# Kernel optimization log

Measured on AMD Instinct MI355X. Metric: run time of the kernel, lower is better.

## Reference

```python
import jax, jax.numpy as jnp
import numpy as np

B = 65536          # batch
NUM_RULES = 4      # num_rules (init default)
NUM_VARS = 2       # effective num_variables after op-slot handling
RULE_DIM = 64
VAR_DIM = 100      # per-variable feature dim
HIDDEN_DIM = 2 * VAR_DIM  # 200, pinned by primary[:, :100] cat -> rule_mlp(hidden_dim)
D_K = 32           # variable_rule_select key dim
MLP_HID = 128      # GroupMLP hidden width


def _uniform(key, shape, fan_in):
    bound = 1.0 / np.sqrt(fan_in)
    return jax.random.uniform(key, shape, minval=-bound, maxval=bound, dtype=jnp.float32)


def setup_inputs() -> dict:
    key = jax.random.key(0)
    ks = jax.random.split(key, 7)
    return {
        "hidden": jax.random.normal(ks[0], (B, 3, VAR_DIM), dtype=jnp.float32),
        # rule embeddings: nn.Parameter(torch.randn(1, num_rules, rule_dim))
        "rule_emb": jax.random.normal(ks[1], (1, NUM_RULES, RULE_DIM), dtype=jnp.float32),
        # SelectAttention shared query (share_query=True -> nn.Linear(rule_dim, d_k))
        "Wq": _uniform(ks[2], (RULE_DIM, D_K), RULE_DIM),
        "bq": _uniform(ks[3], (D_K,), RULE_DIM),
        # SelectAttention per-variable key proj (GroupLinearLayer(hidden_dim, d_k, num_vars))
        "Wk": _uniform(ks[4], (NUM_VARS, HIDDEN_DIM, D_K), HIDDEN_DIM),
        # rule_mlp = GroupMLP(hidden_dim, hidden_dim//2, num_rules): two grouped linears
        "W1": _uniform(ks[5], (NUM_RULES, HIDDEN_DIM, MLP_HID), HIDDEN_DIM),
        "W2": _uniform(ks[6], (NUM_RULES, MLP_HID, VAR_DIM), MLP_HID),
    }


def argmax_onehot(x):
    # ArgMax.forward: scatter 1 at argmax along dim 1 (eval-mode hard selection)
    return jax.nn.one_hot(jnp.argmax(x, axis=1), x.shape[1], dtype=x.dtype)


def reference(hidden, rule_emb, Wq, bq, Wk, W1, W2):
    b = hidden.shape[0]
    # build operand representations: op slot broadcast onto both operands
    op = jnp.repeat(hidden[:, 2:3, :], NUM_VARS, axis=1)            # (B, 2, 100)
    h = jnp.concatenate([hidden[:, :NUM_VARS, :], op], axis=-1)    # (B, 2, 200)

    rule_e = jnp.broadcast_to(rule_emb, (b, NUM_RULES, RULE_DIM))   # (B, 4, 64)

    # SelectAttention(rule_emb, hidden): shared query linear, grouped key linear
    read = rule_e @ Wq + bq                                         # (B, 4, 32)
    write = jnp.einsum('bvd,vdk->bvk', h, Wk)                       # (B, 2, 32)
    scores = jnp.einsum('brk,bvk->brv', read, write) / jnp.sqrt(jnp.float32(D_K))  # (B,4,2)

    # eval path: hard ArgMax one-hot over flattened (rule, variable) pairs
    mask = argmax_onehot(scores.reshape(b, -1)).reshape(b, NUM_RULES, NUM_VARS)
    mask = jnp.transpose(mask, (0, 2, 1))                           # (B, vars, rules)

    variable_mask = jnp.sum(mask, axis=2, keepdims=True)            # (B, 2, 1)
    rule_mask = jnp.sum(mask, axis=1)[:, :, None]                   # (B, 4, 1)

    primary = jnp.sum(h * variable_mask, axis=1)                    # (B, 200)
    context = jnp.sum(h * (1.0 - variable_mask), axis=1)            # (B, 200)

    rule_mlp_input = jnp.concatenate(
        [primary[:, :VAR_DIM], context[:, :VAR_DIM]], axis=1)       # (B, 200)

    # grouped rule MLP applied per rule, then gated by rule_mask
    x = jnp.broadcast_to(rule_mlp_input[:, None, :], (b, NUM_RULES, HIDDEN_DIM))
    x = jax.nn.relu(jnp.einsum('bnd,ndk->bnk', x, W1))              # (B, 4, 128)
    x = jnp.einsum('bnd,ndk->bnk', x, W2)                           # (B, 4, 100)
    out = jnp.sum(x * rule_mask, axis=1)                            # (B, 100)
    return out
```

## Files before the change

kernel.cpp:

```cpp
#include <hip/hip_runtime.h>
#include <hip/hip_bf16.h>

#define B_TOTAL 65536
#define NR 4
#define VD 100
#define HD 200
#define DK 32
#define MH 128
#define RD 64

typedef __attribute__((ext_vector_type(8))) short bf16x8;
typedef __attribute__((ext_vector_type(4))) float f32x4;

static __device__ inline unsigned short f2bf(float x) {
    __hip_bfloat16 h = __float2bfloat16(x);
    return __builtin_bit_cast(unsigned short, h);
}

#define WS_GC    0
#define WS_CNT   19200
#define WS_LIST  19456
#define WS_VB    543744
#define WS_W1F   609280
#define WS_W2F   838656

__global__ __launch_bounds__(256) void k0_prep(
    const float* __restrict__ rule_emb, const float* __restrict__ Wq,
    const float* __restrict__ bq, const float* __restrict__ Wk,
    double* __restrict__ Gc, int* __restrict__ cnt)
{
    int tid = threadIdx.x;
    if (tid < NR) cnt[tid] = 0;

    __shared__ double readS[NR * DK];
    if (tid < NR * DK) {
        int r = tid >> 5, k = tid & 31;
        double a = (double)bq[k];
        for (int d = 0; d < RD; ++d)
            a += (double)rule_emb[r * RD + d] * (double)Wq[d * DK + k];
        readS[tid] = a;
    }
    __syncthreads();

    for (int idx = tid; idx < 100 * 16; idx += 256) {
        int dd = idx >> 4, c = idx & 15;
        int isB = (c >> 3) & 1, v = (c >> 2) & 1, r = c & 3;
        int row = v * HD + isB * 100 + dd;
        double g = 0.0;
        for (int k = 0; k < DK; ++k)
            g += (double)Wk[row * DK + k] * readS[r * DK + k];
        Gc[idx] = g;
    }
}

__global__ __launch_bounds__(256) void k0_wfrag(
    const float* __restrict__ W1, const float* __restrict__ W2,
    unsigned short* __restrict__ W1f, unsigned short* __restrict__ W2f)
{
    int i = blockIdx.x * 256 + threadIdx.x;
    if (i < 114688) {
        int r = i / 28672, rem = i % 28672;
        int ks = rem / 4096, rem2 = rem % 4096;
        int n = rem2 >> 9, l = (rem2 >> 3) & 63, j = rem2 & 7;
        int k = ks * 32 + ((l >> 4) << 3) + j;
        int c = n * 16 + (l & 15);
        float v = (k < HD) ? W1[((size_t)r * HD + k) * MH + c] : 0.f;
        W1f[i] = f2bf(v);
    } else if (i < 114688 + 57344) {
        int t = i - 114688;
        int r = t / 14336, rem = t % 14336;
        int ks = rem / 3584, rem2 = rem % 3584;
        int n = rem2 >> 9, l = (rem2 >> 3) & 63, j = rem2 & 7;
        int k = ks * 32 + ((l >> 4) << 3) + j;
        int c = n * 16 + (l & 15);
        float v = (c < VD) ? W2[((size_t)r * MH + k) * VD + c] : 0.f;
        W2f[t] = f2bf(v);
    }
}

__global__ __launch_bounds__(256) void k1_select(
    const float* __restrict__ hidden, const double* __restrict__ Gc,
    int* __restrict__ cnt, unsigned short* __restrict__ list16,
    unsigned char* __restrict__ vbyte)
{
    __shared__ double Gs[100 * 16];
    __shared__ int lcnt[NR];
    __shared__ int lbase[NR];
    int tid = threadIdx.x;
    for (int i = tid; i < 1600; i += 256) Gs[i] = Gc[i];
    if (tid < NR) lcnt[tid] = 0;
    __syncthreads();

    int b = blockIdx.x * 256 + tid;
    const float4* h0 = (const float4*)(hidden + (size_t)b * 300);
    const float4* h1 = h0 + 25;
    const float4* h2 = h0 + 50;

    double acc[16];
#pragma unroll
    for (int c = 0; c < 16; ++c) acc[c] = 0.0;

    for (int t0 = 0; t0 < 25; t0 += 5) {
        float4 va[5], vb[5], vc[5];
#pragma unroll
        for (int u = 0; u < 5; ++u) { va[u] = h0[t0 + u]; vb[u] = h1[t0 + u]; vc[u] = h2[t0 + u]; }
#pragma unroll
        for (int u = 0; u < 5; ++u) {
            float e0[4] = {va[u].x, va[u].y, va[u].z, va[u].w};
            float e1[4] = {vb[u].x, vb[u].y, vb[u].z, vb[u].w};
            float e2[4] = {vc[u].x, vc[u].y, vc[u].z, vc[u].w};
#pragma unroll
            for (int q = 0; q < 4; ++q) {
                int dd = (t0 + u) * 4 + q;
                const double* g = &Gs[dd * 16];
                double x0 = (double)e0[q], x1 = (double)e1[q], x2 = (double)e2[q];
#pragma unroll
                for (int r = 0; r < 4; ++r) acc[r]     = fma(x0, g[r],     acc[r]);
#pragma unroll
                for (int r = 0; r < 4; ++r) acc[4 + r] = fma(x1, g[4 + r], acc[4 + r]);
#pragma unroll
                for (int r = 0; r < 8; ++r) acc[8 + r] = fma(x2, g[8 + r], acc[8 + r]);
            }
        }
    }

    double sc[8];
#pragma unroll
    for (int r = 0; r < 4; ++r) {
        sc[r * 2]     = acc[r]     + acc[8 + r];
        sc[r * 2 + 1] = acc[4 + r] + acc[12 + r];
    }
    int best = 0; double bv = sc[0];
#pragma unroll
    for (int p = 1; p < 8; ++p) if (sc[p] > bv) { bv = sc[p]; best = p; }
    int r = best >> 1, v = best & 1;

    vbyte[b] = (unsigned char)v;
    int pos = atomicAdd(&lcnt[r], 1);
    __syncthreads();
    if (tid < NR) lbase[tid] = atomicAdd(&cnt[tid], lcnt[tid]);
    __syncthreads();
    list16[r * B_TOTAL + lbase[r] + pos] = (unsigned short)b;
}

__global__ __launch_bounds__(256) void k2_mlp(
    const float* __restrict__ hidden,
    const unsigned short* __restrict__ W1f, const unsigned short* __restrict__ W2f,
    const int* __restrict__ cnt, const unsigned short* __restrict__ list16,
    const unsigned char* __restrict__ vbyte, float* __restrict__ out)
{
    int r = blockIdx.y;
    int nb = cnt[r];
    int m0 = blockIdx.x * 64;
    if (m0 >= nb) return;
    int me = nb - m0; if (me > 64) me = 64;

    __shared__ __align__(16) unsigned short shbuf[64 * 232];
    __shared__ int ent[64];

    int tid = threadIdx.x;
    int wave = tid >> 6, lane = tid & 63;
    int lr = lane & 15, lk = lane >> 4;
    int wrow0 = wave * 16;

    if (tid < 64) {
        int idx = m0 + tid; if (idx > nb - 1) idx = nb - 1;
        int b = list16[r * B_TOTAL + idx];
        int v = vbyte[b];
        ent[tid] = (b << 1) | v;
    }
    __syncthreads();

    {
        int e = tid >> 2, hh = (tid >> 1) & 1, t = tid & 1;
        int en = ent[e];
        int b = en >> 1, v = en & 1;
        int seg = hh ? (1 - v) : v;
        int q0 = t * 12;
        const float4* src = (const float4*)(hidden + (size_t)b * 300 + seg * 100) + q0;
        float4 hv[13];
#pragma unroll
        for (int u = 0; u < 13; ++u) hv[u] = src[u];
#pragma unroll
        for (int u = 0; u < 13; ++u) {
            ushort4 o;
            o.x = f2bf(hv[u].x); o.y = f2bf(hv[u].y);
            o.z = f2bf(hv[u].z); o.w = f2bf(hv[u].w);
            *(ushort4*)&shbuf[e * 232 + (hh * 25 + q0 + u) * 4] = o;
        }
    }
    {
        int row = tid >> 2, part = tid & 3;
        bf16x8 z = {0, 0, 0, 0, 0, 0, 0, 0};
        *(bf16x8*)&shbuf[row * 232 + 200 + part * 8] = z;
    }
    __syncthreads();

    const unsigned short* W1f_r = W1f + (size_t)r * 28672;
    f32x4 acc1[8];
#pragma unroll
    for (int n = 0; n < 8; ++n) acc1[n] = (f32x4){0.f, 0.f, 0.f, 0.f};

#pragma unroll
    for (int ks = 0; ks < 7; ++ks) {
        bf16x8 a0 = *(const bf16x8*)&shbuf[(wrow0 + lr) * 232 + ks * 32 + lk * 8];
#pragma unroll
        for (int n = 0; n < 8; ++n) {
            bf16x8 bfr = *(const bf16x8*)&W1f_r[(size_t)(ks * 8 + n) * 512 + lane * 8];
            acc1[n] = __builtin_amdgcn_mfma_f32_16x16x32_bf16(a0, bfr, acc1[n], 0, 0, 0);
        }
    }

    __syncthreads();

#pragma unroll
    for (int n = 0; n < 8; ++n)
#pragma unroll
        for (int j = 0; j < 4; ++j) {
            float v = fmaxf(acc1[n][j], 0.f);
            int row = wrow0 + lk * 4 + j;
            shbuf[row * 136 + n * 16 + lr] = f2bf(v);
        }
    __syncthreads();

    const unsigned short* W2f_r = W2f + (size_t)r * 14336;
    f32x4 acc2[7];
#pragma unroll
    for (int n = 0; n < 7; ++n) acc2[n] = (f32x4){0.f, 0.f, 0.f, 0.f};

#pragma unroll
    for (int ks = 0; ks < 4; ++ks) {
        bf16x8 a0 = *(const bf16x8*)&shbuf[(wrow0 + lr) * 136 + ks * 32 + lk * 8];
#pragma unroll
        for (int n = 0; n < 7; ++n) {
            bf16x8 bfr = *(const bf16x8*)&W2f_r[(size_t)(ks * 7 + n) * 512 + lane * 8];
            acc2[n] = __builtin_amdgcn_mfma_f32_16x16x32_bf16(a0, bfr, acc2[n], 0, 0, 0);
        }
    }

#pragma unroll
    for (int n = 0; n < 7; ++n) {
        int col = n * 16 + lr;
        if (col < VD) {
#pragma unroll
            for (int j = 0; j < 4; ++j) {
                int e = wrow0 + lk * 4 + j;
                if (e < me) {
                    int b = ent[e] >> 1;
                    out[(size_t)b * VD + col] = acc2[n][j];
                }
            }
        }
    }
}

extern "C" void kernel_launch(void* const* d_in, const int* in_sizes, int n_in,
                              void* d_out, int out_size, void* d_ws, size_t ws_size,
                              hipStream_t stream) {
    (void)in_sizes; (void)n_in; (void)out_size; (void)ws_size;
    const float* hidden   = (const float*)d_in[0];
    const float* rule_emb = (const float*)d_in[1];
    const float* Wq       = (const float*)d_in[2];
    const float* bq       = (const float*)d_in[3];
    const float* Wk       = (const float*)d_in[4];
    const float* W1       = (const float*)d_in[5];
    const float* W2       = (const float*)d_in[6];
    float* out = (float*)d_out;

    char* ws = (char*)d_ws;
    double* Gc             = (double*)(ws + WS_GC);
    int* cnt               = (int*)(ws + WS_CNT);
    unsigned short* list16 = (unsigned short*)(ws + WS_LIST);
    unsigned char* vbyte   = (unsigned char*)(ws + WS_VB);
    unsigned short* W1f    = (unsigned short*)(ws + WS_W1F);
    unsigned short* W2f    = (unsigned short*)(ws + WS_W2F);

    k0_prep<<<1, 256, 0, stream>>>(rule_emb, Wq, bq, Wk, Gc, cnt);
    k0_wfrag<<<672, 256, 0, stream>>>(W1, W2, W1f, W2f);
    k1_select<<<256, 256, 0, stream>>>(hidden, Gc, cnt, list16, vbyte);
    k2_mlp<<<dim3(1024, NR), 256, 0, stream>>>(hidden, W1f, W2f, cnt, list16, vbyte, out);
}
```

Measured before the change: 84.70 us.

## Compute selection scores with FP64 MFMA over LDS-staged hidden rows

The score computation in k1_select moves from per-thread scalar FP64 FMAs to FP64 MFMA (16x16x4). The hidden rows are staged cooperatively into LDS, and the fused key/query matrix is laid out in MFMA B-fragment form by k0_prep. The output-lane mapping of the MFMA is found at runtime with probe MFMAs, and the grid is raised to 1024 blocks of 64 rows. This aims to cut the heavy FP64 ALU work and the uncoalesced per-thread row loads, at the cost of a larger LDS footprint and an extra scatter and argmax pass through shared memory.

After: 93.60 us. 1.11x slower.

```diff
diff --git a/kernel.cpp b/kernel.cpp
--- a/kernel.cpp
+++ b/kernel.cpp
@@ -11,26 +11,45 @@
 
 typedef __attribute__((ext_vector_type(8))) short bf16x8;
 typedef __attribute__((ext_vector_type(4))) float f32x4;
+typedef __attribute__((ext_vector_type(4))) double f64x4;
 
 static __device__ inline unsigned short f2bf(float x) {
     __hip_bfloat16 h = __float2bfloat16(x);
     return __builtin_bit_cast(unsigned short, h);
 }
 
-#define WS_GC    0
-#define WS_CNT   19200
-#define WS_LIST  19456
-#define WS_VB    543744
-#define WS_W1F   609280
-#define WS_W2F   838656
+#define WS_GF    0
+#define WS_PM    38912
+#define WS_PN    39936
+#define WS_CNT   40960
+#define WS_LIST  41472
+#define WS_VB    565760
+#define WS_W1F   631296
+#define WS_W2F   860672
 
 __global__ __launch_bounds__(256) void k0_prep(
     const float* __restrict__ rule_emb, const float* __restrict__ Wq,
     const float* __restrict__ bq, const float* __restrict__ Wk,
-    double* __restrict__ Gc, int* __restrict__ cnt)
+    double* __restrict__ Gf, int* __restrict__ pm, int* __restrict__ pn,
+    int* __restrict__ cnt)
 {
     int tid = threadIdx.x;
     if (tid < NR) cnt[tid] = 0;
+
+    if (tid < 64) {
+        int l = tid;
+        f64x4 z = {0.0, 0.0, 0.0, 0.0};
+        double a1 = ((l >> 4) == 0) ? (double)(l & 15) : 0.0;
+        f64x4 d1 = __builtin_amdgcn_mfma_f64_16x16x4f64(a1, 1.0, z, 0, 0, 0);
+        double a2 = ((l >> 4) == 0) ? 1.0 : 0.0;
+        double b2 = (double)(l & 15);
+        f64x4 d2 = __builtin_amdgcn_mfma_f64_16x16x4f64(a2, b2, z, 0, 0, 0);
+#pragma unroll
+        for (int j = 0; j < 4; ++j) {
+            pm[l * 4 + j] = (int)(d1[j] + 0.5);
+            pn[l * 4 + j] = (int)(d2[j] + 0.5);
+        }
+    }
 
     __shared__ double readS[NR * DK];
     if (tid < NR * DK) {
@@ -42,14 +61,21 @@
     }
     __syncthreads();
 
-    for (int idx = tid; idx < 100 * 16; idx += 256) {
-        int dd = idx >> 4, c = idx & 15;
-        int isB = (c >> 3) & 1, v = (c >> 2) & 1, r = c & 3;
-        int row = v * HD + isB * 100 + dd;
+    for (int i = tid; i < 76 * 64; i += 256) {
+        int ks = i >> 6, l = i & 63;
+        int k = ks * 4 + (l >> 4), c = l & 15;
         double g = 0.0;
-        for (int k = 0; k < DK; ++k)
-            g += (double)Wk[row * DK + k] * readS[r * DK + k];
-        Gc[idx] = g;
+        if (c < 8 && k < 300) {
+            int r = c >> 1, v = c & 1;
+            int wrow = -1;
+            if (k < 100)        { if (v == 0) wrow = k; }
+            else if (k < 200)   { if (v == 1) wrow = 200 + (k - 100); }
+            else                { wrow = v * 200 + 100 + (k - 200); }
+            if (wrow >= 0)
+                for (int kk = 0; kk < DK; ++kk)
+                    g += (double)Wk[wrow * DK + kk] * readS[r * DK + kk];
+        }
+        Gf[i] = g;
     }
 }
 
@@ -79,68 +105,71 @@
 }
 
 __global__ __launch_bounds__(256) void k1_select(
-    const float* __restrict__ hidden, const double* __restrict__ Gc,
+    const float* __restrict__ hidden, const double* __restrict__ Gf,
+    const int* __restrict__ pm, const int* __restrict__ pn,
     int* __restrict__ cnt, unsigned short* __restrict__ list16,
     unsigned char* __restrict__ vbyte)
 {
-    __shared__ double Gs[100 * 16];
+    __shared__ float hs[64 * 308];
+    __shared__ double scf[64][9];
     __shared__ int lcnt[NR];
     __shared__ int lbase[NR];
     int tid = threadIdx.x;
-    for (int i = tid; i < 1600; i += 256) Gs[i] = Gc[i];
     if (tid < NR) lcnt[tid] = 0;
-    __syncthreads();
-
-    int b = blockIdx.x * 256 + tid;
-    const float4* h0 = (const float4*)(hidden + (size_t)b * 300);
-    const float4* h1 = h0 + 25;
-    const float4* h2 = h0 + 50;
-
-    double acc[16];
-#pragma unroll
-    for (int c = 0; c < 16; ++c) acc[c] = 0.0;
-
-    for (int t0 = 0; t0 < 25; t0 += 5) {
-        float4 va[5], vb[5], vc[5];
-#pragma unroll
-        for (int u = 0; u < 5; ++u) { va[u] = h0[t0 + u]; vb[u] = h1[t0 + u]; vc[u] = h2[t0 + u]; }
-#pragma unroll
-        for (int u = 0; u < 5; ++u) {
-            float e0[4] = {va[u].x, va[u].y, va[u].z, va[u].w};
-            float e1[4] = {vb[u].x, vb[u].y, vb[u].z, vb[u].w};
-            float e2[4] = {vc[u].x, vc[u].y, vc[u].z, vc[u].w};
-#pragma unroll
-            for (int q = 0; q < 4; ++q) {
-                int dd = (t0 + u) * 4 + q;
-                const double* g = &Gs[dd * 16];
-                double x0 = (double)e0[q], x1 = (double)e1[q], x2 = (double)e2[q];
-#pragma unroll
-                for (int r = 0; r < 4; ++r) acc[r]     = fma(x0, g[r],     acc[r]);
-#pragma unroll
-                for (int r = 0; r < 4; ++r) acc[4 + r] = fma(x1, g[4 + r], acc[4 + r]);
-#pragma unroll
-                for (int r = 0; r < 8; ++r) acc[8 + r] = fma(x2, g[8 + r], acc[8 + r]);
-            }
-        }
-    }
-
-    double sc[8];
-#pragma unroll
-    for (int r = 0; r < 4; ++r) {
-        sc[r * 2]     = acc[r]     + acc[8 + r];
-        sc[r * 2 + 1] = acc[4 + r] + acc[12 + r];
-    }
-    int best = 0; double bv = sc[0];
-#pragma unroll
-    for (int p = 1; p < 8; ++p) if (sc[p] > bv) { bv = sc[p]; best = p; }
-    int r = best >> 1, v = best & 1;
-
-    vbyte[b] = (unsigned char)v;
-    int pos = atomicAdd(&lcnt[r], 1);
+
+    int rowbase = blockIdx.x * 64;
+
+    const float4* src4 = (const float4*)(hidden + (size_t)rowbase * 300);
+#pragma unroll
+    for (int k = 0; k < 19; ++k) {
+        int idx = tid + k * 256;
+        if (idx < 4800) {
+            int row = idx / 75, c4 = idx - row * 75;
+            *(float4*)&hs[row * 308 + c4 * 4] = src4[idx];
+        }
+    }
+    if (tid < 128) {
+        int row = tid >> 1, part = tid & 1;
+        *(float4*)&hs[row * 308 + 300 + part * 4] = make_float4(0.f, 0.f, 0.f, 0.f);
+    }
+    __syncthreads();
+
+    int lane = tid & 63, wave = tid >> 6;
+    int arow = wave * 16 + (lane & 15);
+    int klane = lane >> 4;
+
+    f64x4 acc = {0.0, 0.0, 0.0, 0.0};
+#pragma unroll 4
+    for (int ks = 0; ks < 76; ++ks) {
+        double a = (double)hs[arow * 308 + ks * 4 + klane];
+        double b = Gf[ks * 64 + lane];
+        acc = __builtin_amdgcn_mfma_f64_16x16x4f64(a, b, acc, 0, 0, 0);
+    }
+
+#pragma unroll
+    for (int j = 0; j < 4; ++j) {
+        int m = pm[lane * 4 + j];
+        int n = pn[lane * 4 + j];
+        if (n < 8) scf[wave * 16 + m][n] = acc[j];
+    }
+    __syncthreads();
+
+    int r = 0, v = 0, pos = 0;
+    if (tid < 64) {
+        double bv = scf[tid][0]; int best = 0;
+#pragma unroll
+        for (int p = 1; p < 8; ++p) {
+            double s = scf[tid][p];
+            if (s > bv) { bv = s; best = p; }
+        }
+        r = best >> 1; v = best & 1;
+        vbyte[rowbase + tid] = (unsigned char)v;
+        pos = atomicAdd(&lcnt[r], 1);
+    }
     __syncthreads();
     if (tid < NR) lbase[tid] = atomicAdd(&cnt[tid], lcnt[tid]);
     __syncthreads();
-    list16[r * B_TOTAL + lbase[r] + pos] = (unsigned short)b;
+    if (tid < 64) list16[r * B_TOTAL + lbase[r] + pos] = (unsigned short)(rowbase + tid);
 }
 
 __global__ __launch_bounds__(256) void k2_mlp(
@@ -268,15 +297,17 @@
     float* out = (float*)d_out;
 
     char* ws = (char*)d_ws;
-    double* Gc             = (double*)(ws + WS_GC);
+    double* Gf             = (double*)(ws + WS_GF);
+    int* pm                = (int*)(ws + WS_PM);
+    int* pn                = (int*)(ws + WS_PN);
     int* cnt               = (int*)(ws + WS_CNT);
     unsigned short* list16 = (unsigned short*)(ws + WS_LIST);
     unsigned char* vbyte   = (unsigned char*)(ws + WS_VB);
     unsigned short* W1f    = (unsigned short*)(ws + WS_W1F);
     unsigned short* W2f    = (unsigned short*)(ws + WS_W2F);
 
-    k0_prep<<<1, 256, 0, stream>>>(rule_emb, Wq, bq, Wk, Gc, cnt);
+    k0_prep<<<1, 256, 0, stream>>>(rule_emb, Wq, bq, Wk, Gf, pm, pn, cnt);
     k0_wfrag<<<672, 256, 0, stream>>>(W1, W2, W1f, W2f);
-    k1_select<<<256, 256, 0, stream>>>(hidden, Gc, cnt, list16, vbyte);
+    k1_select<<<1024, 256, 0, stream>>>(hidden, Gf, pm, pn, cnt, list16, vbyte);
     k2_mlp<<<dim3(1024, NR), 256, 0, stream>>>(hidden, W1f, W2f, cnt, list16, vbyte, out);
 }
```

## Fuse selection and rule MLP into one kernel with MFMA scoring and fp64 fallback

Applied to the files above, without the earlier changes.

Merges the select and MLP kernels into a single kernel that loads each 64-row tile of hidden once into LDS as bf16. Scores are computed with bf16 MFMA, and only rows whose top-two margin is small are recomputed in fp64 to keep the argmax exact. It drops the global per-rule bucketing (atomics, index lists, scattered gathers). In exchange every tile runs the MLP for all four rules and masks the stores, so MLP MFMA work is four times larger.

Measured after the change: 131.1 us. +54.7%, slower.

```diff
diff --git a/kernel.cpp b/kernel.cpp
--- a/kernel.cpp
+++ b/kernel.cpp
@@ -17,21 +17,17 @@
     return __builtin_bit_cast(unsigned short, h);
 }
 
-#define WS_GC    0
-#define WS_CNT   19200
-#define WS_LIST  19456
-#define WS_VB    543744
-#define WS_W1F   609280
-#define WS_W2F   838656
+#define WS_GD    0
+#define WS_GSC   19200
+#define WS_W1F   30720
+#define WS_W2F   260096
 
 __global__ __launch_bounds__(256) void k0_prep(
     const float* __restrict__ rule_emb, const float* __restrict__ Wq,
     const float* __restrict__ bq, const float* __restrict__ Wk,
-    double* __restrict__ Gc, int* __restrict__ cnt)
+    double* __restrict__ Gd, unsigned short* __restrict__ Gsc)
 {
     int tid = threadIdx.x;
-    if (tid < NR) cnt[tid] = 0;
-
     __shared__ double readS[NR * DK];
     if (tid < NR * DK) {
         int r = tid >> 5, k = tid & 31;
@@ -42,14 +38,39 @@
     }
     __syncthreads();
 
-    for (int idx = tid; idx < 100 * 16; idx += 256) {
-        int dd = idx >> 4, c = idx & 15;
-        int isB = (c >> 3) & 1, v = (c >> 2) & 1, r = c & 3;
-        int row = v * HD + isB * 100 + dd;
+    for (int idx = tid; idx < 2400; idx += 256) {
+        int j = idx >> 3, p = idx & 7;
+        int rr = p >> 1, vv = p & 1;
+        int s = j / 100, dd = j - s * 100;
         double g = 0.0;
-        for (int k = 0; k < DK; ++k)
-            g += (double)Wk[row * DK + k] * readS[r * DK + k];
-        Gc[idx] = g;
+        if (s == vv) {
+            for (int kk = 0; kk < DK; ++kk)
+                g += (double)Wk[(vv * HD + dd) * DK + kk] * readS[rr * DK + kk];
+        } else if (s == 2) {
+            for (int kk = 0; kk < DK; ++kk)
+                g += (double)Wk[(vv * HD + 100 + dd) * DK + kk] * readS[rr * DK + kk];
+        }
+        Gd[idx] = g;
+    }
+
+    for (int i = tid; i < 11 * 512; i += 256) {
+        int ks = i >> 9, l = (i >> 3) & 63, j = i & 7;
+        int k = ks * 32 + ((l >> 4) << 3) + j;
+        int p = l & 15;
+        double g = 0.0;
+        if (p < 8 && k < 336) {
+            int seg = k / 112, dd = k - seg * 112;
+            if (dd < 100) {
+                int rr = p >> 1, vv = p & 1;
+                int wrow = -1;
+                if (seg == vv)      wrow = vv * HD + dd;
+                else if (seg == 2)  wrow = vv * HD + 100 + dd;
+                if (wrow >= 0)
+                    for (int kk = 0; kk < DK; ++kk)
+                        g += (double)Wk[wrow * DK + kk] * readS[rr * DK + kk];
+            }
+        }
+        Gsc[i] = f2bf((float)g);
     }
 }
 
@@ -64,7 +85,8 @@
         int n = rem2 >> 9, l = (rem2 >> 3) & 63, j = rem2 & 7;
         int k = ks * 32 + ((l >> 4) << 3) + j;
         int c = n * 16 + (l & 15);
-        float v = (k < HD) ? W1[((size_t)r * HD + k) * MH + c] : 0.f;
+        int kp = (k < 100) ? k : (k >= 112 && k < 212) ? (k - 12) : -1;
+        float v = (kp >= 0) ? W1[((size_t)r * HD + kp) * MH + c] : 0.f;
         W1f[i] = f2bf(v);
     } else if (i < 114688 + 57344) {
         int t = i - 114688;
@@ -78,176 +100,156 @@
     }
 }
 
-__global__ __launch_bounds__(256) void k1_select(
-    const float* __restrict__ hidden, const double* __restrict__ Gc,
-    int* __restrict__ cnt, unsigned short* __restrict__ list16,
-    unsigned char* __restrict__ vbyte)
+__global__ __launch_bounds__(256) void k_main(
+    const float* __restrict__ hidden, const unsigned short* __restrict__ Gsc,
+    const double* __restrict__ Gd, const unsigned short* __restrict__ W1f,
+    const unsigned short* __restrict__ W2f, float* __restrict__ out)
 {
-    __shared__ double Gs[100 * 16];
-    __shared__ int lcnt[NR];
-    __shared__ int lbase[NR];
+    __shared__ __align__(16) unsigned short hb[64 * 360];
+    __shared__ __align__(16) unsigned short c1[64 * 136];
+    __shared__ int vr[64], rs[64];
+    __shared__ int flagl[64];
+    __shared__ int nflag;
+
     int tid = threadIdx.x;
-    for (int i = tid; i < 1600; i += 256) Gs[i] = Gc[i];
-    if (tid < NR) lcnt[tid] = 0;
-    __syncthreads();
-
-    int b = blockIdx.x * 256 + tid;
-    const float4* h0 = (const float4*)(hidden + (size_t)b * 300);
-    const float4* h1 = h0 + 25;
-    const float4* h2 = h0 + 50;
-
-    double acc[16];
-#pragma unroll
-    for (int c = 0; c < 16; ++c) acc[c] = 0.0;
-
-    for (int t0 = 0; t0 < 25; t0 += 5) {
-        float4 va[5], vb[5], vc[5];
-#pragma unroll
-        for (int u = 0; u < 5; ++u) { va[u] = h0[t0 + u]; vb[u] = h1[t0 + u]; vc[u] = h2[t0 + u]; }
-#pragma unroll
-        for (int u = 0; u < 5; ++u) {
-            float e0[4] = {va[u].x, va[u].y, va[u].z, va[u].w};
-            float e1[4] = {vb[u].x, vb[u].y, vb[u].z, vb[u].w};
-            float e2[4] = {vc[u].x, vc[u].y, vc[u].z, vc[u].w};
-#pragma unroll
-            for (int q = 0; q < 4; ++q) {
-                int dd = (t0 + u) * 4 + q;
-                const double* g = &Gs[dd * 16];
-                double x0 = (double)e0[q], x1 = (double)e1[q], x2 = (double)e2[q];
-#pragma unroll
-                for (int r = 0; r < 4; ++r) acc[r]     = fma(x0, g[r],     acc[r]);
-#pragma unroll
-                for (int r = 0; r < 4; ++r) acc[4 + r] = fma(x1, g[4 + r], acc[4 + r]);
-#pragma unroll
-                for (int r = 0; r < 8; ++r) acc[8 + r] = fma(x2, g[8 + r], acc[8 + r]);
-            }
-        }
-    }
-
-    double sc[8];
-#pragma unroll
-    for (int r = 0; r < 4; ++r) {
-        sc[r * 2]     = acc[r]     + acc[8 + r];
-        sc[r * 2 + 1] = acc[4 + r] + acc[12 + r];
-    }
-    int best = 0; double bv = sc[0];
-#pragma unroll
-    for (int p = 1; p < 8; ++p) if (sc[p] > bv) { bv = sc[p]; best = p; }
-    int r = best >> 1, v = best & 1;
-
-    vbyte[b] = (unsigned char)v;
-    int pos = atomicAdd(&lcnt[r], 1);
-    __syncthreads();
-    if (tid < NR) lbase[tid] = atomicAdd(&cnt[tid], lcnt[tid]);
-    __syncthreads();
-    list16[r * B_TOTAL + lbase[r] + pos] = (unsigned short)b;
-}
-
-__global__ __launch_bounds__(256) void k2_mlp(
-    const float* __restrict__ hidden,
-    const unsigned short* __restrict__ W1f, const unsigned short* __restrict__ W2f,
-    const int* __restrict__ cnt, const unsigned short* __restrict__ list16,
-    const unsigned char* __restrict__ vbyte, float* __restrict__ out)
-{
-    int r = blockIdx.y;
-    int nb = cnt[r];
-    int m0 = blockIdx.x * 64;
-    if (m0 >= nb) return;
-    int me = nb - m0; if (me > 64) me = 64;
-
-    __shared__ __align__(16) unsigned short shbuf[64 * 232];
-    __shared__ int ent[64];
-
-    int tid = threadIdx.x;
+    int rowbase = blockIdx.x * 64;
+    if (tid == 0) nflag = 0;
+
+    const float4* src4 = (const float4*)(hidden + (size_t)rowbase * 300);
+#pragma unroll
+    for (int kk = 0; kk < 19; ++kk) {
+        int idx = tid + kk * 256;
+        if (idx < 4800) {
+            int row = idx / 75, c4 = idx - row * 75;
+            float4 v = src4[idx];
+            int cg = c4 * 4, seg = cg / 100, dd = cg - seg * 100;
+            ushort4 o;
+            o.x = f2bf(v.x); o.y = f2bf(v.y); o.z = f2bf(v.z); o.w = f2bf(v.w);
+            *(ushort4*)&hb[row * 360 + seg * 112 + dd] = o;
+        }
+    }
+    for (int i = tid; i < 960; i += 256) {
+        int row = i / 15, t = i - (i / 15) * 15;
+        int off = (t < 3) ? (100 + t * 4) : (t < 6) ? (212 + (t - 3) * 4) : (324 + (t - 6) * 4);
+        ushort4 z; z.x = z.y = z.z = z.w = 0;
+        *(ushort4*)&hb[row * 360 + off] = z;
+    }
+    __syncthreads();
+
     int wave = tid >> 6, lane = tid & 63;
     int lr = lane & 15, lk = lane >> 4;
     int wrow0 = wave * 16;
 
-    if (tid < 64) {
-        int idx = m0 + tid; if (idx > nb - 1) idx = nb - 1;
-        int b = list16[r * B_TOTAL + idx];
-        int v = vbyte[b];
-        ent[tid] = (b << 1) | v;
-    }
-    __syncthreads();
-
     {
-        int e = tid >> 2, hh = (tid >> 1) & 1, t = tid & 1;
-        int en = ent[e];
-        int b = en >> 1, v = en & 1;
-        int seg = hh ? (1 - v) : v;
-        int q0 = t * 12;
-        const float4* src = (const float4*)(hidden + (size_t)b * 300 + seg * 100) + q0;
-        float4 hv[13];
-#pragma unroll
-        for (int u = 0; u < 13; ++u) hv[u] = src[u];
-#pragma unroll
-        for (int u = 0; u < 13; ++u) {
-            ushort4 o;
-            o.x = f2bf(hv[u].x); o.y = f2bf(hv[u].y);
-            o.z = f2bf(hv[u].z); o.w = f2bf(hv[u].w);
-            *(ushort4*)&shbuf[e * 232 + (hh * 25 + q0 + u) * 4] = o;
-        }
-    }
+        f32x4 sacc = (f32x4){0.f, 0.f, 0.f, 0.f};
+#pragma unroll
+        for (int ks = 0; ks < 11; ++ks) {
+            bf16x8 a = *(const bf16x8*)&hb[(wrow0 + lr) * 360 + ks * 32 + lk * 8];
+            bf16x8 g = *(const bf16x8*)&Gsc[(size_t)ks * 512 + lane * 8];
+            sacc = __builtin_amdgcn_mfma_f32_16x16x32_bf16(a, g, sacc, 0, 0, 0);
+        }
+#pragma unroll
+        for (int j = 0; j < 4; ++j) {
+            float v1 = (lr < 8) ? sacc[j] : -3.4e38f;
+            int i1 = lr;
+            float v2 = -3.4e38f;
+#pragma unroll
+            for (int m = 1; m <= 8; m <<= 1) {
+                float ov1 = __shfl_xor(v1, m);
+                int oi1 = __shfl_xor(i1, m);
+                float ov2 = __shfl_xor(v2, m);
+                float nv2 = fmaxf(fminf(v1, ov1), fmaxf(v2, ov2));
+                if (ov1 > v1 || (ov1 == v1 && oi1 < i1)) { v1 = ov1; i1 = oi1; }
+                v2 = nv2;
+            }
+            if (lr == 0) {
+                int row = wrow0 + lk * 4 + j;
+                vr[row] = i1 & 1; rs[row] = i1 >> 1;
+                if (v1 - v2 < 0.5f) { int s = atomicAdd(&nflag, 1); flagl[s] = row; }
+            }
+        }
+    }
+    __syncthreads();
+
+    for (int f = wave; f < nflag; f += 4) {
+        int row = flagl[f];
+        const float* hr = hidden + (size_t)(rowbase + row) * 300;
+        double a8[8];
+#pragma unroll
+        for (int p = 0; p < 8; ++p) a8[p] = 0.0;
+        for (int e = lane; e < 300; e += 64) {
+            double x = (double)hr[e];
+#pragma unroll
+            for (int p = 0; p < 8; ++p) a8[p] = fma(x, Gd[e * 8 + p], a8[p]);
+        }
+#pragma unroll
+        for (int m = 1; m < 64; m <<= 1)
+#pragma unroll
+            for (int p = 0; p < 8; ++p) a8[p] += __shfl_xor(a8[p], m);
+        if (lane == 0) {
+            double bv = a8[0]; int best = 0;
+#pragma unroll
+            for (int p = 1; p < 8; ++p) if (a8[p] > bv) { bv = a8[p]; best = p; }
+            vr[row] = best & 1; rs[row] = best >> 1;
+        }
+    }
+    __syncthreads();
+
+    int myv = 0;
     {
-        int row = tid >> 2, part = tid & 3;
-        bf16x8 z = {0, 0, 0, 0, 0, 0, 0, 0};
-        *(bf16x8*)&shbuf[row * 232 + 200 + part * 8] = z;
-    }
-    __syncthreads();
-
-    const unsigned short* W1f_r = W1f + (size_t)r * 28672;
-    f32x4 acc1[8];
-#pragma unroll
-    for (int n = 0; n < 8; ++n) acc1[n] = (f32x4){0.f, 0.f, 0.f, 0.f};
-
-#pragma unroll
-    for (int ks = 0; ks < 7; ++ks) {
-        bf16x8 a0 = *(const bf16x8*)&shbuf[(wrow0 + lr) * 232 + ks * 32 + lk * 8];
-#pragma unroll
-        for (int n = 0; n < 8; ++n) {
-            bf16x8 bfr = *(const bf16x8*)&W1f_r[(size_t)(ks * 8 + n) * 512 + lane * 8];
-            acc1[n] = __builtin_amdgcn_mfma_f32_16x16x32_bf16(a0, bfr, acc1[n], 0, 0, 0);
-        }
-    }
-
-    __syncthreads();
-
-#pragma unroll
-    for (int n = 0; n < 8; ++n)
-#pragma unroll
-        for (int j = 0; j < 4; ++j) {
-            float v = fmaxf(acc1[n][j], 0.f);
-            int row = wrow0 + lk * 4 + j;
-            shbuf[row * 136 + n * 16 + lr] = f2bf(v);
-        }
-    __syncthreads();
-
-    const unsigned short* W2f_r = W2f + (size_t)r * 14336;
-    f32x4 acc2[7];
-#pragma unroll
-    for (int n = 0; n < 7; ++n) acc2[n] = (f32x4){0.f, 0.f, 0.f, 0.f};
-
-#pragma unroll
-    for (int ks = 0; ks < 4; ++ks) {
-        bf16x8 a0 = *(const bf16x8*)&shbuf[(wrow0 + lr) * 136 + ks * 32 + lk * 8];
+        myv = vr[wrow0 + lr];
+    }
+    for (int r = 0; r < NR; ++r) {
+        const unsigned short* W1f_r = W1f + (size_t)r * 28672;
+        f32x4 acc1[8];
+#pragma unroll
+        for (int n = 0; n < 8; ++n) acc1[n] = (f32x4){0.f, 0.f, 0.f, 0.f};
+
+#pragma unroll
+        for (int ks = 0; ks < 7; ++ks) {
+            int c0 = ks * 32 + lk * 8;
+            int addr = (c0 < 112) ? ((wrow0 + lr) * 360 + myv * 112 + c0)
+                                  : ((wrow0 + lr) * 360 + (1 - myv) * 112 + (c0 - 112));
+            bf16x8 a0 = *(const bf16x8*)&hb[addr];
+#pragma unroll
+            for (int n = 0; n < 8; ++n) {
+                bf16x8 bfr = *(const bf16x8*)&W1f_r[(size_t)(ks * 8 + n) * 512 + lane * 8];
+                acc1[n] = __builtin_amdgcn_mfma_f32_16x16x32_bf16(a0, bfr, acc1[n], 0, 0, 0);
+            }
+        }
+
+#pragma unroll
+        for (int n = 0; n < 8; ++n)
+#pragma unroll
+            for (int j = 0; j < 4; ++j) {
+                float v = fmaxf(acc1[n][j], 0.f);
+                c1[(wrow0 + lk * 4 + j) * 136 + n * 16 + lr] = f2bf(v);
+            }
+
+        const unsigned short* W2f_r = W2f + (size_t)r * 14336;
+        f32x4 acc2[7];
+#pragma unroll
+        for (int n = 0; n < 7; ++n) acc2[n] = (f32x4){0.f, 0.f, 0.f, 0.f};
+
+#pragma unroll
+        for (int ks = 0; ks < 4; ++ks) {
+            bf16x8 a0 = *(const bf16x8*)&c1[(wrow0 + lr) * 136 + ks * 32 + lk * 8];
+#pragma unroll
+            for (int n = 0; n < 7; ++n) {
+                bf16x8 bfr = *(const bf16x8*)&W2f_r[(size_t)(ks * 7 + n) * 512 + lane * 8];
+                acc2[n] = __builtin_amdgcn_mfma_f32_16x16x32_bf16(a0, bfr, acc2[n], 0, 0, 0);
+            }
+        }
+
 #pragma unroll
         for (int n = 0; n < 7; ++n) {
-            bf16x8 bfr = *(const bf16x8*)&W2f_r[(size_t)(ks * 7 + n) * 512 + lane * 8];
-            acc2[n] = __builtin_amdgcn_mfma_f32_16x16x32_bf16(a0, bfr, acc2[n], 0, 0, 0);
-        }
-    }
-
-#pragma unroll
-    for (int n = 0; n < 7; ++n) {
-        int col = n * 16 + lr;
-        if (col < VD) {
-#pragma unroll
-            for (int j = 0; j < 4; ++j) {
-                int e = wrow0 + lk * 4 + j;
-                if (e < me) {
-                    int b = ent[e] >> 1;
-                    out[(size_t)b * VD + col] = acc2[n][j];
+            int col = n * 16 + lr;
+            if (col < VD) {
+#pragma unroll
+                for (int j = 0; j < 4; ++j) {
+                    int e = wrow0 + lk * 4 + j;
+                    if (rs[e] == r)
+                        out[(size_t)(rowbase + e) * VD + col] = acc2[n][j];
                 }
             }
         }
@@ -268,15 +270,12 @@
     float* out = (float*)d_out;
 
     char* ws = (char*)d_ws;
-    double* Gc             = (double*)(ws + WS_GC);
-    int* cnt               = (int*)(ws + WS_CNT);
-    unsigned short* list16 = (unsigned short*)(ws + WS_LIST);
-    unsigned char* vbyte   = (unsigned char*)(ws + WS_VB);
-    unsigned short* W1f    = (unsigned short*)(ws + WS_W1F);
-    unsigned short* W2f    = (unsigned short*)(ws + WS_W2F);
-
-    k0_prep<<<1, 256, 0, stream>>>(rule_emb, Wq, bq, Wk, Gc, cnt);
+    double* Gd            = (double*)(ws + WS_GD);
+    unsigned short* Gsc   = (unsigned short*)(ws + WS_GSC);
+    unsigned short* W1f   = (unsigned short*)(ws + WS_W1F);
+    unsigned short* W2f   = (unsigned short*)(ws + WS_W2F);
+
+    k0_prep<<<1, 256, 0, stream>>>(rule_emb, Wq, bq, Wk, Gd, Gsc);
     k0_wfrag<<<672, 256, 0, stream>>>(W1, W2, W1f, W2f);
-    k1_select<<<256, 256, 0, stream>>>(hidden, Gc, cnt, list16, vbyte);
-    k2_mlp<<<dim3(1024, NR), 256, 0, stream>>>(hidden, W1f, W2f, cnt, list16, vbyte, out);
-}
+    k_main<<<1024, 256, 0, stream>>>(hidden, Gsc, Gd, W1f, W2f, out);
+}
```
